# Performance work log

Measured on AMD Instinct MI355X. Metric: run time of the kernel, lower is better.

## Reference

```python
import jax, jax.numpy as jnp
import numpy as np

B, T, IN, H, OUT = 16384, 200, 9, 64, 3


def setup_inputs() -> dict:
    key = jax.random.key(0)
    ks = jax.random.split(key, 12)
    s_in, s_h = 1.0 / np.sqrt(H), 1.0 / np.sqrt(H)  # torch LSTMCell init scale = 1/sqrt(hidden)
    u = lambda k, shape: jax.random.uniform(k, shape, jnp.float32, -s_h, s_h)
    return {
        "x": jax.random.normal(ks[0], (B, T, IN), jnp.float32),
        "W_ih1": u(ks[1], (4 * H, IN)),
        "W_hh1": u(ks[2], (4 * H, H)),
        "b_ih1": u(ks[3], (4 * H,)),
        "b_hh1": u(ks[4], (4 * H,)),
        "W_ih2": u(ks[5], (4 * H, H)),
        "W_hh2": u(ks[6], (4 * H, H)),
        "b_ih2": u(ks[7], (4 * H,)),
        "b_hh2": u(ks[8], (4 * H,)),
        "W_out": u(ks[9], (OUT, H)),
        "b_out": u(ks[10], (OUT,)),
    }


def _lstm_cell(x, h, c, W_ih, W_hh, b_ih, b_hh):
    # PyTorch gate order: i, f, g, o
    gates = x @ W_ih.T + b_ih + h @ W_hh.T + b_hh  # [B, 4H]
    i, f, g, o = jnp.split(gates, 4, axis=-1)
    i, f, o = jax.nn.sigmoid(i), jax.nn.sigmoid(f), jax.nn.sigmoid(o)
    g = jnp.tanh(g)
    c_new = f * c + i * g
    h_new = o * jnp.tanh(c_new)
    return h_new, c_new


def reference(x, W_ih1, W_hh1, b_ih1, b_hh1, W_ih2, W_hh2, b_ih2, b_hh2, W_out, b_out):
    batch = x.shape[0]
    hdim = W_hh1.shape[1]
    zeros = jnp.zeros((batch, hdim), x.dtype)
    init = (zeros, zeros, zeros, zeros)  # h1, c1, h2, c2

    def step(carry, x_t):
        h1, c1, h2, c2 = carry
        h1, c1 = _lstm_cell(x_t, h1, c1, W_ih1, W_hh1, b_ih1, b_hh1)
        h2, c2 = _lstm_cell(h1, h2, c2, W_ih2, W_hh2, b_ih2, b_hh2)
        return (h1, c1, h2, c2), None

    (h1, c1, h2, c2), _ = jax.lax.scan(step, init, jnp.swapaxes(x, 0, 1))  # scan over time
    out = h2 @ W_out.T + b_out  # [B, OUT]
    return out[:, None, :]  # [B, 1, OUT]
```

## Files before the change

### kernel.cpp

```cpp
#include <hip/hip_runtime.h>
#include <hip/hip_bf16.h>


#define B_TOT   16384
#define T_STEPS 200
#define IN_DIM  9
#define HDIM    64

#define PK1_OFF 0
#define PK2_OFF 24576
#define BSUM_HALF_OFF 57344
#define PACK_W_TOT 57344
#define PACK_TOT (PACK_W_TOT + 512)

#define L2E     1.44269504089f
#define TWOL2E  2.88539008178f

typedef _Float16 half8  __attribute__((ext_vector_type(8)));
typedef _Float16 half4v __attribute__((ext_vector_type(4)));
typedef float    f32x4  __attribute__((ext_vector_type(4)));
typedef float    f4u    __attribute__((ext_vector_type(4), aligned(4)));

__global__ void pack_kernel(const float* __restrict__ Wih1, const float* __restrict__ Whh1,
                            const float* __restrict__ bih1, const float* __restrict__ bhh1,
                            const float* __restrict__ Wih2, const float* __restrict__ Whh2,
                            const float* __restrict__ bih2, const float* __restrict__ bhh2,
                            float* __restrict__ ws) {
    int e = blockIdx.x * 256 + threadIdx.x;
    if (e >= PACK_TOT) return;
    _Float16* wh = (_Float16*)ws;
    float* bptr = (float*)(wh + BSUM_HALF_OFF);
    auto gscale = [](int q) -> float {
        int gt = q >> 6;
        return (gt == 2) ? (-2.0f * L2E) : -L2E;
    };
    if (e < PK2_OFF) {
        int j = e & 7, lane = (e >> 3) & 63, nt = (e >> 9) & 15, c = e >> 13;
        int k = c * 32 + 4 * (lane >> 4) + (j & 3) + 16 * (j >> 2);
        int q = nt * 16 + (lane & 15);
        float v = 0.0f;
        if (k < 64)      v = Whh1[q * 64 + k];
        else if (k < 73) v = Wih1[q * 9 + (k - 64)];
        wh[e] = (_Float16)(v * gscale(q));
    } else if (e < PACK_W_TOT) {
        int e2 = e - PK2_OFF;
        int j = e2 & 7, lane = (e2 >> 3) & 63, nt = (e2 >> 9) & 15, c = e2 >> 13;
        int k = c * 32 + 4 * (lane >> 4) + (j & 3) + 16 * (j >> 2);
        int q = nt * 16 + (lane & 15);
        float v = (k < 64) ? Wih2[q * 64 + k] : Whh2[q * 64 + (k - 64)];
        wh[e] = (_Float16)(v * gscale(q));
    } else if (e < PACK_W_TOT + 256) {
        int q = e - PACK_W_TOT;
        bptr[q] = (bih1[q] + bhh1[q]) * gscale(q);
    } else {
        int q = e - PACK_W_TOT - 256;
        bptr[256 + q] = (bih2[q] + bhh2[q]) * gscale(q);
    }
}

__global__ __launch_bounds__(256, 2) void lstm_mfma(
    const float* __restrict__ x,
    const float* __restrict__ ws_f,
    const float* __restrict__ Wout,
    const float* __restrict__ bout,
    float* __restrict__ out)
{
    const int tid  = threadIdx.x;
    const int lane = tid & 63;
    const int w    = __builtin_amdgcn_readfirstlane(tid >> 6);
    const int l15  = lane & 15;
    const int l4   = lane >> 4;

    const _Float16* wh  = (const _Float16*)ws_f;
    const _Float16* pk1 = wh + PK1_OFF;
    const _Float16* pk2 = wh + PK2_OFF;
    const float* bsum   = (const float*)(wh + BSUM_HALF_OFF);

    __shared__ _Float16 h1s[2][16][72];
    __shared__ _Float16 h2s[2][16][72];
    __shared__ _Float16 xwin[2][8][4][16][4];

    for (int i = tid; i < 2 * 16 * 72; i += 256) {
        (&h1s[0][0][0])[i] = (_Float16)0.0f;
        (&h2s[0][0][0])[i] = (_Float16)0.0f;
    }
    for (int i = tid; i < 2 * 8 * 4 * 16 * 4; i += 256)
        (&xwin[0][0][0][0][0])[i] = (_Float16)0.0f;

    const int bbase = blockIdx.x * 16;

    const int b_ = tid & 15, z_ = tid >> 4;
    const int s0_ = (z_ * 11) >> 5, q0_ = z_ - 3 * s0_;
    const bool act1 = (z_ < 8);
    const int pz1 = z_ + 16;
    const int s1_ = (pz1 * 11) >> 5, q1_ = pz1 - 3 * s1_;
    const float* xbL = x + (long)(bbase + b_) * (T_STEPS * IN_DIM);

    f4u pfA = {0.f, 0.f, 0.f, 0.f}, pfB = {0.f, 0.f, 0.f, 0.f};
    auto fetch_x = [&](int wb) {
        int t0 = wb + s0_; if (t0 > T_STEPS - 1) t0 = T_STEPS - 1;
        const float* p0 = xbL + t0 * IN_DIM + 4 * q0_;
        if (q0_ < 2) pfA = *(const f4u*)p0; else pfA[0] = p0[0];
        if (act1) {
            int t1 = wb + s1_; if (t1 > T_STEPS - 1) t1 = T_STEPS - 1;
            const float* p1 = xbL + t1 * IN_DIM + 4 * q1_;
            if (q1_ < 2) pfB = *(const f4u*)p1; else pfB[0] = p1[0];
        }
    };
    auto store_x = [&](int buf) {
        f4u A = pfA, B = pfB;
        if (q0_ == 2) { A[1] = 0.f; A[2] = 0.f; A[3] = 0.f; }
        half4v hv;
        hv[0] = (_Float16)A[0]; hv[1] = (_Float16)A[1];
        hv[2] = (_Float16)A[2]; hv[3] = (_Float16)A[3];
        *(half4v*)&xwin[buf][s0_][q0_][b_][0] = hv;
        if (act1) {
            if (q1_ == 2) { B[1] = 0.f; B[2] = 0.f; B[3] = 0.f; }
            half4v hw;
            hw[0] = (_Float16)B[0]; hw[1] = (_Float16)B[1];
            hw[2] = (_Float16)B[2]; hw[3] = (_Float16)B[3];
            *(half4v*)&xwin[buf][s1_][q1_][b_][0] = hw;
        }
    };
    auto read_ax = [&](int tt) -> half8 {
        half4v xq = *(const half4v*)&xwin[(tt >> 3) & 1][tt & 7][l4][l15][0];
        return __builtin_shufflevector(xq, xq, 0, 1, 2, 3, 0, 1, 2, 3);
    };

    half8 bw1_00, bw1_01, bw1_02, bw1_03;
    half8 bw1_10, bw1_11, bw1_12, bw1_13;
    half8 bw1_20, bw1_21, bw1_22, bw1_23;
    half8 bw2_00, bw2_01, bw2_02, bw2_03;
    half8 bw2_10, bw2_11, bw2_12, bw2_13;
    half8 bw2_20, bw2_21, bw2_22, bw2_23;
    half8 bw2_30, bw2_31, bw2_32, bw2_33;
    {
        #define LD1(c,g) *(const half8*)(pk1 + (((c * 16) + (w + 4 * g)) * 64 + lane) * 8)
        #define LD2(c,g) *(const half8*)(pk2 + (((c * 16) + (w + 4 * g)) * 64 + lane) * 8)
        bw1_00 = LD1(0,0); bw1_01 = LD1(0,1); bw1_02 = LD1(0,2); bw1_03 = LD1(0,3);
        bw1_10 = LD1(1,0); bw1_11 = LD1(1,1); bw1_12 = LD1(1,2); bw1_13 = LD1(1,3);
        bw1_20 = LD1(2,0); bw1_21 = LD1(2,1); bw1_22 = LD1(2,2); bw1_23 = LD1(2,3);
        bw2_00 = LD2(0,0); bw2_01 = LD2(0,1); bw2_02 = LD2(0,2); bw2_03 = LD2(0,3);
        bw2_10 = LD2(1,0); bw2_11 = LD2(1,1); bw2_12 = LD2(1,2); bw2_13 = LD2(1,3);
        bw2_20 = LD2(2,0); bw2_21 = LD2(2,1); bw2_22 = LD2(2,2); bw2_23 = LD2(2,3);
        bw2_30 = LD2(3,0); bw2_31 = LD2(3,1); bw2_32 = LD2(3,2); bw2_33 = LD2(3,3);
        #undef LD1
        #undef LD2
    }

    float bias1[4], bias2[4];
    #pragma unroll
    for (int g = 0; g < 4; ++g) {
        bias1[g] = bsum[(w + 4 * g) * 16 + l15];
        bias2[g] = bsum[256 + (w + 4 * g) * 16 + l15];
    }

    const int hpos = ((w >> 1) << 5) + 8 * (l15 >> 2) + (l15 & 3) + ((w & 1) << 2);

    f32x4 c1 = {0.f, 0.f, 0.f, 0.f};
    f32x4 c2 = {0.f, 0.f, 0.f, 0.f};

    auto cell_update = [&](f32x4* G, f32x4& cs, _Float16* hb) {
        float num[4], den[4], eo4[4], d2[4], hs4[4];
        #pragma unroll
        for (int r = 0; r < 4; ++r) {
            float ei = __builtin_amdgcn_exp2f(G[0][r]);
            float ef = __builtin_amdgcn_exp2f(G[1][r]);
            float eg = __builtin_amdgcn_exp2f(G[2][r]);
            eo4[r]   = __builtin_amdgcn_exp2f(G[3][r]);
            float ai = 1.0f + ei, af = 1.0f + ef, ag = 1.0f + eg;
            float gm = 1.0f - eg;
            float pp = ai * ag;
            num[r] = __builtin_fmaf(gm, af, cs[r] * pp);
            den[r] = af * pp;
        }
        float s01 = den[0] * den[1], s23 = den[2] * den[3];
        float Pinv = __builtin_amdgcn_rcpf(s01 * s23);
        float r01 = Pinv * s23, r23 = Pinv * s01;
        float inv0 = r01 * den[1], inv1 = r01 * den[0];
        float inv2 = r23 * den[3], inv3 = r23 * den[2];
        float inv[4] = {inv0, inv1, inv2, inv3};
        #pragma unroll
        for (int r = 0; r < 4; ++r) {
            float cc = num[r] * inv[r];
            cs[r] = cc;
            float z  = cc * TWOL2E;
            int   zi = __float_as_int(z);
            float ec = __builtin_amdgcn_exp2f(__int_as_float(zi | (int)0x80000000));
            float tm = 1.0f - ec;
            d2[r] = (1.0f + eo4[r]) * (1.0f + ec);
            hs4[r] = __int_as_float(__float_as_int(tm) ^ (zi & (int)0x80000000));
        }
        float t01 = d2[0] * d2[1], t23 = d2[2] * d2[3];
        float Qinv = __builtin_amdgcn_rcpf(t01 * t23);
        float q01 = Qinv * t23, q23 = Qinv * t01;
        float jnv[4] = {q01 * d2[1], q01 * d2[0], q23 * d2[3], q23 * d2[2]};
        #pragma unroll
        for (int r = 0; r < 4; ++r)
            hb[(4 * l4 + r) * 72 + hpos] = (_Float16)(hs4[r] * jnv[r]);
    };

    #define PIN_ALL() do {                                                      \
        asm volatile("" :                                                       \
            "+v"(bw1_00), "+v"(bw1_01), "+v"(bw1_02), "+v"(bw1_03),             \
            "+v"(bw1_10), "+v"(bw1_11), "+v"(bw1_12), "+v"(bw1_13),             \
            "+v"(bw1_20), "+v"(bw1_21), "+v"(bw1_22), "+v"(bw1_23));            \
        asm volatile("" :                                                       \
            "+v"(bw2_00), "+v"(bw2_01), "+v"(bw2_02), "+v"(bw2_03),             \
            "+v"(bw2_10), "+v"(bw2_11), "+v"(bw2_12), "+v"(bw2_13),             \
            "+v"(bw2_20), "+v"(bw2_21), "+v"(bw2_22), "+v"(bw2_23),             \
            "+v"(bw2_30), "+v"(bw2_31), "+v"(bw2_32), "+v"(bw2_33),             \
            "+v"(bias1[0]), "+v"(bias1[1]), "+v"(bias1[2]), "+v"(bias1[3]),     \
            "+v"(bias2[0]), "+v"(bias2[1]), "+v"(bias2[2]), "+v"(bias2[3]));    \
    } while (0)

    fetch_x(0);
    __syncthreads();
    store_x(0);
    fetch_x(8);
    __syncthreads();

    f32x4 C[4];
    {
        half8 ax0 = read_ax(0);
        #pragma unroll
        for (int g = 0; g < 4; ++g) C[g] = (f32x4){bias1[g], bias1[g], bias1[g], bias1[g]};
        C[0] = __builtin_amdgcn_mfma_f32_16x16x32_f16(ax0, bw1_20, C[0], 0, 0, 0);
        C[1] = __builtin_amdgcn_mfma_f32_16x16x32_f16(ax0, bw1_21, C[1], 0, 0, 0);
        C[2] = __builtin_amdgcn_mfma_f32_16x16x32_f16(ax0, bw1_22, C[2], 0, 0, 0);
        C[3] = __builtin_amdgcn_mfma_f32_16x16x32_f16(ax0, bw1_23, C[3], 0, 0, 0);
    }

    for (int t = 0; t < T_STEPS; t += 2) {
        PIN_ALL();
        cell_update(C, c1, &h1s[1][0][0]);
        if ((t & 7) == 0) {
            store_x(((t >> 3) + 1) & 1);
            fetch_x(t + 16);
        }
        __syncthreads();

        half8 a10  = *(const half8*)&h1s[1][l15][ 0 + 8 * l4];
        half8 a11  = *(const half8*)&h1s[1][l15][32 + 8 * l4];
        half8 a2h0 = *(const half8*)&h2s[0][l15][ 0 + 8 * l4];
        half8 a2h1 = *(const half8*)&h2s[0][l15][32 + 8 * l4];
        half8 ax   = read_ax(t + 1);

        f32x4 D[4];
        #pragma unroll
        for (int g = 0; g < 4; ++g) D[g] = (f32x4){bias2[g], bias2[g], bias2[g], bias2[g]};
        D[0] = __builtin_amdgcn_mfma_f32_16x16x32_f16(a10,  bw2_00, D[0], 0, 0, 0);
        D[1] = __builtin_amdgcn_mfma_f32_16x16x32_f16(a10,  bw2_01, D[1], 0, 0, 0);
        D[2] = __builtin_amdgcn_mfma_f32_16x16x32_f16(a10,  bw2_02, D[2], 0, 0, 0);
        D[3] = __builtin_amdgcn_mfma_f32_16x16x32_f16(a10,  bw2_03, D[3], 0, 0, 0);
        D[0] = __builtin_amdgcn_mfma_f32_16x16x32_f16(a11,  bw2_10, D[0], 0, 0, 0);
        D[1] = __builtin_amdgcn_mfma_f32_16x16x32_f16(a11,  bw2_11, D[1], 0, 0, 0);
        D[2] = __builtin_amdgcn_mfma_f32_16x16x32_f16(a11,  bw2_12, D[2], 0, 0, 0);
        D[3] = __builtin_amdgcn_mfma_f32_16x16x32_f16(a11,  bw2_13, D[3], 0, 0, 0);
        D[0] = __builtin_amdgcn_mfma_f32_16x16x32_f16(a2h0, bw2_20, D[0], 0, 0, 0);
        D[1] = __builtin_amdgcn_mfma_f32_16x16x32_f16(a2h0, bw2_21, D[1], 0, 0, 0);
        D[2] = __builtin_amdgcn_mfma_f32_16x16x32_f16(a2h0, bw2_22, D[2], 0, 0, 0);
        D[3] = __builtin_amdgcn_mfma_f32_16x16x32_f16(a2h0, bw2_23, D[3], 0, 0, 0);
        D[0] = __builtin_amdgcn_mfma_f32_16x16x32_f16(a2h1, bw2_30, D[0], 0, 0, 0);
        D[1] = __builtin_amdgcn_mfma_f32_16x16x32_f16(a2h1, bw2_31, D[1], 0, 0, 0);
        D[2] = __builtin_amdgcn_mfma_f32_16x16x32_f16(a2h1, bw2_32, D[2], 0, 0, 0);
        D[3] = __builtin_amdgcn_mfma_f32_16x16x32_f16(a2h1, bw2_33, D[3], 0, 0, 0);

        f32x4 CB[4];
        #pragma unroll
        for (int g = 0; g < 4; ++g) CB[g] = (f32x4){bias1[g], bias1[g], bias1[g], bias1[g]};
        CB[0] = __builtin_amdgcn_mfma_f32_16x16x32_f16(a10, bw1_00, CB[0], 0, 0, 0);
        CB[1] = __builtin_amdgcn_mfma_f32_16x16x32_f16(a10, bw1_01, CB[1], 0, 0, 0);
        CB[2] = __builtin_amdgcn_mfma_f32_16x16x32_f16(a10, bw1_02, CB[2], 0, 0, 0);
        CB[3] = __builtin_amdgcn_mfma_f32_16x16x32_f16(a10, bw1_03, CB[3], 0, 0, 0);
        CB[0] = __builtin_amdgcn_mfma_f32_16x16x32_f16(a11, bw1_10, CB[0], 0, 0, 0);
        CB[1] = __builtin_amdgcn_mfma_f32_16x16x32_f16(a11, bw1_11, CB[1], 0, 0, 0);
        CB[2] = __builtin_amdgcn_mfma_f32_16x16x32_f16(a11, bw1_12, CB[2], 0, 0, 0);
        CB[3] = __builtin_amdgcn_mfma_f32_16x16x32_f16(a11, bw1_13, CB[3], 0, 0, 0);
        CB[0] = __builtin_amdgcn_mfma_f32_16x16x32_f16(ax,  bw1_20, CB[0], 0, 0, 0);
        CB[1] = __builtin_amdgcn_mfma_f32_16x16x32_f16(ax,  bw1_21, CB[1], 0, 0, 0);
        CB[2] = __builtin_amdgcn_mfma_f32_16x16x32_f16(ax,  bw1_22, CB[2], 0, 0, 0);
        CB[3] = __builtin_amdgcn_mfma_f32_16x16x32_f16(ax,  bw1_23, CB[3], 0, 0, 0);

        cell_update(D, c2, &h2s[1][0][0]);

        PIN_ALL();
        cell_update(CB, c1, &h1s[0][0][0]);
        __syncthreads();

        half8 b10  = *(const half8*)&h1s[0][l15][ 0 + 8 * l4];
        half8 b11  = *(const half8*)&h1s[0][l15][32 + 8 * l4];
        half8 b2h0 = *(const half8*)&h2s[1][l15][ 0 + 8 * l4];
        half8 b2h1 = *(const half8*)&h2s[1][l15][32 + 8 * l4];
        half8 bx   = read_ax(t + 2);

        f32x4 E[4];
        #pragma unroll
        for (int g = 0; g < 4; ++g) E[g] = (f32x4){bias2[g], bias2[g], bias2[g], bias2[g]};
        E[0] = __builtin_amdgcn_mfma_f32_16x16x32_f16(b10,  bw2_00, E[0], 0, 0, 0);
        E[1] = __builtin_amdgcn_mfma_f32_16x16x32_f16(b10,  bw2_01, E[1], 0, 0, 0);
        E[2] = __builtin_amdgcn_mfma_f32_16x16x32_f16(b10,  bw2_02, E[2], 0, 0, 0);
        E[3] = __builtin_amdgcn_mfma_f32_16x16x32_f16(b10,  bw2_03, E[3], 0, 0, 0);
        E[0] = __builtin_amdgcn_mfma_f32_16x16x32_f16(b11,  bw2_10, E[0], 0, 0, 0);
        E[1] = __builtin_amdgcn_mfma_f32_16x16x32_f16(b11,  bw2_11, E[1], 0, 0, 0);
        E[2] = __builtin_amdgcn_mfma_f32_16x16x32_f16(b11,  bw2_12, E[2], 0, 0, 0);
        E[3] = __builtin_amdgcn_mfma_f32_16x16x32_f16(b11,  bw2_13, E[3], 0, 0, 0);
        E[0] = __builtin_amdgcn_mfma_f32_16x16x32_f16(b2h0, bw2_20, E[0], 0, 0, 0);
        E[1] = __builtin_amdgcn_mfma_f32_16x16x32_f16(b2h0, bw2_21, E[1], 0, 0, 0);
        E[2] = __builtin_amdgcn_mfma_f32_16x16x32_f16(b2h0, bw2_22, E[2], 0, 0, 0);
        E[3] = __builtin_amdgcn_mfma_f32_16x16x32_f16(b2h0, bw2_23, E[3], 0, 0, 0);
        E[0] = __builtin_amdgcn_mfma_f32_16x16x32_f16(b2h1, bw2_30, E[0], 0, 0, 0);
        E[1] = __builtin_amdgcn_mfma_f32_16x16x32_f16(b2h1, bw2_31, E[1], 0, 0, 0);
        E[2] = __builtin_amdgcn_mfma_f32_16x16x32_f16(b2h1, bw2_32, E[2], 0, 0, 0);
        E[3] = __builtin_amdgcn_mfma_f32_16x16x32_f16(b2h1, bw2_33, E[3], 0, 0, 0);

        #pragma unroll
        for (int g = 0; g < 4; ++g) C[g] = (f32x4){bias1[g], bias1[g], bias1[g], bias1[g]};
        C[0] = __builtin_amdgcn_mfma_f32_16x16x32_f16(b10, bw1_00, C[0], 0, 0, 0);
        C[1] = __builtin_amdgcn_mfma_f32_16x16x32_f16(b10, bw1_01, C[1], 0, 0, 0);
        C[2] = __builtin_amdgcn_mfma_f32_16x16x32_f16(b10, bw1_02, C[2], 0, 0, 0);
        C[3] = __builtin_amdgcn_mfma_f32_16x16x32_f16(b10, bw1_03, C[3], 0, 0, 0);
        C[0] = __builtin_amdgcn_mfma_f32_16x16x32_f16(b11, bw1_10, C[0], 0, 0, 0);
        C[1] = __builtin_amdgcn_mfma_f32_16x16x32_f16(b11, bw1_11, C[1], 0, 0, 0);
        C[2] = __builtin_amdgcn_mfma_f32_16x16x32_f16(b11, bw1_12, C[2], 0, 0, 0);
        C[3] = __builtin_amdgcn_mfma_f32_16x16x32_f16(b11, bw1_13, C[3], 0, 0, 0);
        C[0] = __builtin_amdgcn_mfma_f32_16x16x32_f16(bx,  bw1_20, C[0], 0, 0, 0);
        C[1] = __builtin_amdgcn_mfma_f32_16x16x32_f16(bx,  bw1_21, C[1], 0, 0, 0);
        C[2] = __builtin_amdgcn_mfma_f32_16x16x32_f16(bx,  bw1_22, C[2], 0, 0, 0);
        C[3] = __builtin_amdgcn_mfma_f32_16x16x32_f16(bx,  bw1_23, C[3], 0, 0, 0);

        cell_update(E, c2, &h2s[0][0][0]);
    }
    __syncthreads();

    if (tid < 48) {
        int bl = tid / 3, o = tid - bl * 3;
        float acc = bout[o];
        #pragma unroll 8
        for (int pos = 0; pos < HDIM; ++pos) {
            int sub = pos & 31;
            int j = (pos >> 5) * 32 + (((sub >> 2) & 1) << 4) + ((sub >> 3) << 2) + (sub & 3);
            acc = __builtin_fmaf(Wout[o * 64 + j], (float)h2s[0][bl][pos], acc);
        }
        out[(bbase + bl) * 3 + o] = acc;
    }
    #undef PIN_ALL
}

extern "C" void kernel_launch(void* const* d_in, const int* in_sizes, int n_in,
                              void* d_out, int out_size, void* d_ws, size_t ws_size,
                              hipStream_t stream) {
    const float* x     = (const float*)d_in[0];
    const float* Wih1  = (const float*)d_in[1];
    const float* Whh1  = (const float*)d_in[2];
    const float* bih1  = (const float*)d_in[3];
    const float* bhh1  = (const float*)d_in[4];
    const float* Wih2  = (const float*)d_in[5];
    const float* Whh2  = (const float*)d_in[6];
    const float* bih2  = (const float*)d_in[7];
    const float* bhh2  = (const float*)d_in[8];
    const float* Wout  = (const float*)d_in[9];
    const float* bout  = (const float*)d_in[10];
    float* ws  = (float*)d_ws;
    float* out = (float*)d_out;

    pack_kernel<<<(PACK_TOT + 255) / 256, 256, 0, stream>>>(
        Wih1, Whh1, bih1, bhh1, Wih2, Whh2, bih2, bhh2, ws);

    lstm_mfma<<<B_TOT / 16, 256, 0, stream>>>(x, ws, Wout, bout, out);
}
```

Baseline: 526.4 us.

## Process two independent 16-row batch tiles per block to interleave recurrences

Each block now handles 32 batch rows as two independent 16-row tiles (P and Q) with separate shared-memory state. Their MFMA chains and cell updates are interleaved so one tile's latency-bound recurrence overlaps the other's. The weights held in registers are shared by both tiles, which halves the grid size and the per-row barrier count. s_setprio is also raised around the MFMA sections. The cost is more registers and LDS per block and fewer blocks to spread across CUs, which may reduce occupancy.

```diff
diff --git a/kernel.cpp b/kernel.cpp
--- a/kernel.cpp
+++ b/kernel.cpp
@@ -76,54 +76,58 @@
     const _Float16* pk2 = wh + PK2_OFF;
     const float* bsum   = (const float*)(wh + BSUM_HALF_OFF);
 
-    __shared__ _Float16 h1s[2][16][72];
-    __shared__ _Float16 h2s[2][16][72];
-    __shared__ _Float16 xwin[2][8][4][16][4];
+    __shared__ _Float16 h1P[2][16][72], h2P[2][16][72];
+    __shared__ _Float16 h1Q[2][16][72], h2Q[2][16][72];
+    __shared__ _Float16 xwP[2][8][4][16][4], xwQ[2][8][4][16][4];
 
     for (int i = tid; i < 2 * 16 * 72; i += 256) {
-        (&h1s[0][0][0])[i] = (_Float16)0.0f;
-        (&h2s[0][0][0])[i] = (_Float16)0.0f;
-    }
-    for (int i = tid; i < 2 * 8 * 4 * 16 * 4; i += 256)
-        (&xwin[0][0][0][0][0])[i] = (_Float16)0.0f;
-
-    const int bbase = blockIdx.x * 16;
+        (&h1P[0][0][0])[i] = (_Float16)0.0f; (&h2P[0][0][0])[i] = (_Float16)0.0f;
+        (&h1Q[0][0][0])[i] = (_Float16)0.0f; (&h2Q[0][0][0])[i] = (_Float16)0.0f;
+    }
+    for (int i = tid; i < 2 * 8 * 4 * 16 * 4; i += 256) {
+        (&xwP[0][0][0][0][0])[i] = (_Float16)0.0f;
+        (&xwQ[0][0][0][0][0])[i] = (_Float16)0.0f;
+    }
+
+    const int bbase = blockIdx.x * 32;
 
     const int b_ = tid & 15, z_ = tid >> 4;
     const int s0_ = (z_ * 11) >> 5, q0_ = z_ - 3 * s0_;
     const bool act1 = (z_ < 8);
     const int pz1 = z_ + 16;
     const int s1_ = (pz1 * 11) >> 5, q1_ = pz1 - 3 * s1_;
-    const float* xbL = x + (long)(bbase + b_) * (T_STEPS * IN_DIM);
-
-    f4u pfA = {0.f, 0.f, 0.f, 0.f}, pfB = {0.f, 0.f, 0.f, 0.f};
-    auto fetch_x = [&](int wb) {
+    const float* xbP = x + (long)(bbase + b_) * (T_STEPS * IN_DIM);
+    const float* xbQ = x + (long)(bbase + 16 + b_) * (T_STEPS * IN_DIM);
+
+    f4u pfPA = {0.f,0.f,0.f,0.f}, pfPB = {0.f,0.f,0.f,0.f};
+    f4u pfQA = {0.f,0.f,0.f,0.f}, pfQB = {0.f,0.f,0.f,0.f};
+
+    auto fetch_t = [&](const float* xb, f4u& A, f4u& B, int wb) {
         int t0 = wb + s0_; if (t0 > T_STEPS - 1) t0 = T_STEPS - 1;
-        const float* p0 = xbL + t0 * IN_DIM + 4 * q0_;
-        if (q0_ < 2) pfA = *(const f4u*)p0; else pfA[0] = p0[0];
+        const float* p0 = xb + t0 * IN_DIM + 4 * q0_;
+        if (q0_ < 2) A = *(const f4u*)p0; else A[0] = p0[0];
         if (act1) {
             int t1 = wb + s1_; if (t1 > T_STEPS - 1) t1 = T_STEPS - 1;
-            const float* p1 = xbL + t1 * IN_DIM + 4 * q1_;
-            if (q1_ < 2) pfB = *(const f4u*)p1; else pfB[0] = p1[0];
-        }
-    };
-    auto store_x = [&](int buf) {
-        f4u A = pfA, B = pfB;
+            const float* p1 = xb + t1 * IN_DIM + 4 * q1_;
+            if (q1_ < 2) B = *(const f4u*)p1; else B[0] = p1[0];
+        }
+    };
+    auto store_t = [&](_Float16 (*xw)[8][4][16][4], f4u A, f4u B, int buf) {
         if (q0_ == 2) { A[1] = 0.f; A[2] = 0.f; A[3] = 0.f; }
         half4v hv;
         hv[0] = (_Float16)A[0]; hv[1] = (_Float16)A[1];
         hv[2] = (_Float16)A[2]; hv[3] = (_Float16)A[3];
-        *(half4v*)&xwin[buf][s0_][q0_][b_][0] = hv;
+        *(half4v*)&xw[buf][s0_][q0_][b_][0] = hv;
         if (act1) {
             if (q1_ == 2) { B[1] = 0.f; B[2] = 0.f; B[3] = 0.f; }
             half4v hw;
             hw[0] = (_Float16)B[0]; hw[1] = (_Float16)B[1];
             hw[2] = (_Float16)B[2]; hw[3] = (_Float16)B[3];
-            *(half4v*)&xwin[buf][s1_][q1_][b_][0] = hw;
-        }
-    };
-    auto read_ax = [&](int tt) -> half8 {
-        half4v xq = *(const half4v*)&xwin[(tt >> 3) & 1][tt & 7][l4][l15][0];
+            *(half4v*)&xw[buf][s1_][q1_][b_][0] = hw;
+        }
+    };
+    auto read_ax = [&](const _Float16 (*xw)[8][4][16][4], int tt) -> half8 {
+        half4v xq = *(const half4v*)&xw[(tt >> 3) & 1][tt & 7][l4][l15][0];
         return __builtin_shufflevector(xq, xq, 0, 1, 2, 3, 0, 1, 2, 3);
     };
 
@@ -157,8 +161,8 @@
 
     const int hpos = ((w >> 1) << 5) + 8 * (l15 >> 2) + (l15 & 3) + ((w & 1) << 2);
 
-    f32x4 c1 = {0.f, 0.f, 0.f, 0.f};
-    f32x4 c2 = {0.f, 0.f, 0.f, 0.f};
+    f32x4 c1P = {0.f,0.f,0.f,0.f}, c2P = {0.f,0.f,0.f,0.f};
+    f32x4 c1Q = {0.f,0.f,0.f,0.f}, c2Q = {0.f,0.f,0.f,0.f};
 
     auto cell_update = [&](f32x4* G, f32x4& cs, _Float16* hb) {
         float num[4], den[4], eo4[4], d2[4], hs4[4];
@@ -177,9 +181,7 @@
         float s01 = den[0] * den[1], s23 = den[2] * den[3];
         float Pinv = __builtin_amdgcn_rcpf(s01 * s23);
         float r01 = Pinv * s23, r23 = Pinv * s01;
-        float inv0 = r01 * den[1], inv1 = r01 * den[0];
-        float inv2 = r23 * den[3], inv3 = r23 * den[2];
-        float inv[4] = {inv0, inv1, inv2, inv3};
+        float inv[4] = {r01 * den[1], r01 * den[0], r23 * den[3], r23 * den[2]};
         #pragma unroll
         for (int r = 0; r < 4; ++r) {
             float cc = num[r] * inv[r];
@@ -198,6 +200,43 @@
         #pragma unroll
         for (int r = 0; r < 4; ++r)
             hb[(4 * l4 + r) * 72 + hpos] = (_Float16)(hs4[r] * jnv[r]);
+    };
+
+    auto initb = [&](f32x4* A, const float* b) {
+        #pragma unroll
+        for (int g = 0; g < 4; ++g) A[g] = (f32x4){b[g], b[g], b[g], b[g]};
+    };
+    auto L2C = [&](f32x4* D, half8 u0, half8 u1, half8 v0, half8 v1) {
+        D[0] = __builtin_amdgcn_mfma_f32_16x16x32_f16(u0, bw2_00, D[0], 0, 0, 0);
+        D[1] = __builtin_amdgcn_mfma_f32_16x16x32_f16(u0, bw2_01, D[1], 0, 0, 0);
+        D[2] = __builtin_amdgcn_mfma_f32_16x16x32_f16(u0, bw2_02, D[2], 0, 0, 0);
+        D[3] = __builtin_amdgcn_mfma_f32_16x16x32_f16(u0, bw2_03, D[3], 0, 0, 0);
+        D[0] = __builtin_amdgcn_mfma_f32_16x16x32_f16(u1, bw2_10, D[0], 0, 0, 0);
+        D[1] = __builtin_amdgcn_mfma_f32_16x16x32_f16(u1, bw2_11, D[1], 0, 0, 0);
+        D[2] = __builtin_amdgcn_mfma_f32_16x16x32_f16(u1, bw2_12, D[2], 0, 0, 0);
+        D[3] = __builtin_amdgcn_mfma_f32_16x16x32_f16(u1, bw2_13, D[3], 0, 0, 0);
+        D[0] = __builtin_amdgcn_mfma_f32_16x16x32_f16(v0, bw2_20, D[0], 0, 0, 0);
+        D[1] = __builtin_amdgcn_mfma_f32_16x16x32_f16(v0, bw2_21, D[1], 0, 0, 0);
+        D[2] = __builtin_amdgcn_mfma_f32_16x16x32_f16(v0, bw2_22, D[2], 0, 0, 0);
+        D[3] = __builtin_amdgcn_mfma_f32_16x16x32_f16(v0, bw2_23, D[3], 0, 0, 0);
+        D[0] = __builtin_amdgcn_mfma_f32_16x16x32_f16(v1, bw2_30, D[0], 0, 0, 0);
+        D[1] = __builtin_amdgcn_mfma_f32_16x16x32_f16(v1, bw2_31, D[1], 0, 0, 0);
+        D[2] = __builtin_amdgcn_mfma_f32_16x16x32_f16(v1, bw2_32, D[2], 0, 0, 0);
+        D[3] = __builtin_amdgcn_mfma_f32_16x16x32_f16(v1, bw2_33, D[3], 0, 0, 0);
+    };
+    auto L1C = [&](f32x4* C, half8 u0, half8 u1, half8 axm) {
+        C[0] = __builtin_amdgcn_mfma_f32_16x16x32_f16(u0, bw1_00, C[0], 0, 0, 0);
+        C[1] = __builtin_amdgcn_mfma_f32_16x16x32_f16(u0, bw1_01, C[1], 0, 0, 0);
+        C[2] = __builtin_amdgcn_mfma_f32_16x16x32_f16(u0, bw1_02, C[2], 0, 0, 0);
+        C[3] = __builtin_amdgcn_mfma_f32_16x16x32_f16(u0, bw1_03, C[3], 0, 0, 0);
+        C[0] = __builtin_amdgcn_mfma_f32_16x16x32_f16(u1, bw1_10, C[0], 0, 0, 0);
+        C[1] = __builtin_amdgcn_mfma_f32_16x16x32_f16(u1, bw1_11, C[1], 0, 0, 0);
+        C[2] = __builtin_amdgcn_mfma_f32_16x16x32_f16(u1, bw1_12, C[2], 0, 0, 0);
+        C[3] = __builtin_amdgcn_mfma_f32_16x16x32_f16(u1, bw1_13, C[3], 0, 0, 0);
+        C[0] = __builtin_amdgcn_mfma_f32_16x16x32_f16(axm, bw1_20, C[0], 0, 0, 0);
+        C[1] = __builtin_amdgcn_mfma_f32_16x16x32_f16(axm, bw1_21, C[1], 0, 0, 0);
+        C[2] = __builtin_amdgcn_mfma_f32_16x16x32_f16(axm, bw1_22, C[2], 0, 0, 0);
+        C[3] = __builtin_amdgcn_mfma_f32_16x16x32_f16(axm, bw1_23, C[3], 0, 0, 0);
     };
 
     #define PIN_ALL() do {                                                      \
@@ -214,133 +253,112 @@
             "+v"(bias2[0]), "+v"(bias2[1]), "+v"(bias2[2]), "+v"(bias2[3]));    \
     } while (0)
 
-    fetch_x(0);
+    fetch_t(xbP, pfPA, pfPB, 0);
+    fetch_t(xbQ, pfQA, pfQB, 0);
     __syncthreads();
-    store_x(0);
-    fetch_x(8);
+    store_t(xwP, pfPA, pfPB, 0);
+    store_t(xwQ, pfQA, pfQB, 0);
+    fetch_t(xbP, pfPA, pfPB, 8);
+    fetch_t(xbQ, pfQA, pfQB, 8);
     __syncthreads();
 
-    f32x4 C[4];
+    f32x4 CP[4], CQ[4];
     {
-        half8 ax0 = read_ax(0);
-        #pragma unroll
-        for (int g = 0; g < 4; ++g) C[g] = (f32x4){bias1[g], bias1[g], bias1[g], bias1[g]};
-        C[0] = __builtin_amdgcn_mfma_f32_16x16x32_f16(ax0, bw1_20, C[0], 0, 0, 0);
-        C[1] = __builtin_amdgcn_mfma_f32_16x16x32_f16(ax0, bw1_21, C[1], 0, 0, 0);
-        C[2] = __builtin_amdgcn_mfma_f32_16x16x32_f16(ax0, bw1_22, C[2], 0, 0, 0);
-        C[3] = __builtin_amdgcn_mfma_f32_16x16x32_f16(ax0, bw1_23, C[3], 0, 0, 0);
+        half8 ax0 = read_ax(xwP, 0);
+        initb(CP, bias1);
+        CP[0] = __builtin_amdgcn_mfma_f32_16x16x32_f16(ax0, bw1_20, CP[0], 0, 0, 0);
+        CP[1] = __builtin_amdgcn_mfma_f32_16x16x32_f16(ax0, bw1_21, CP[1], 0, 0, 0);
+        CP[2] = __builtin_amdgcn_mfma_f32_16x16x32_f16(ax0, bw1_22, CP[2], 0, 0, 0);
+        CP[3] = __builtin_amdgcn_mfma_f32_16x16x32_f16(ax0, bw1_23, CP[3], 0, 0, 0);
+        half8 ax1 = read_ax(xwQ, 0);
+        initb(CQ, bias1);
+        CQ[0] = __builtin_amdgcn_mfma_f32_16x16x32_f16(ax1, bw1_20, CQ[0], 0, 0, 0);
+        CQ[1] = __builtin_amdgcn_mfma_f32_16x16x32_f16(ax1, bw1_21, CQ[1], 0, 0, 0);
+        CQ[2] = __builtin_amdgcn_mfma_f32_16x16x32_f16(ax1, bw1_22, CQ[2], 0, 0, 0);
+        CQ[3] = __builtin_amdgcn_mfma_f32_16x16x32_f16(ax1, bw1_23, CQ[3], 0, 0, 0);
     }
 
     for (int t = 0; t < T_STEPS; t += 2) {
         PIN_ALL();
-        cell_update(C, c1, &h1s[1][0][0]);
+        cell_update(CP, c1P, &h1P[1][0][0]);
+        cell_update(CQ, c1Q, &h1Q[1][0][0]);
         if ((t & 7) == 0) {
-            store_x(((t >> 3) + 1) & 1);
-            fetch_x(t + 16);
+            int nb = ((t >> 3) + 1) & 1;
+            store_t(xwP, pfPA, pfPB, nb);
+            store_t(xwQ, pfQA, pfQB, nb);
+            fetch_t(xbP, pfPA, pfPB, t + 16);
+            fetch_t(xbQ, pfQA, pfQB, t + 16);
         }
         __syncthreads();
-
-        half8 a10  = *(const half8*)&h1s[1][l15][ 0 + 8 * l4];
-        half8 a11  = *(const half8*)&h1s[1][l15][32 + 8 * l4];
-        half8 a2h0 = *(const half8*)&h2s[0][l15][ 0 + 8 * l4];
-        half8 a2h1 = *(const half8*)&h2s[0][l15][32 + 8 * l4];
-        half8 ax   = read_ax(t + 1);
-
-        f32x4 D[4];
-        #pragma unroll
-        for (int g = 0; g < 4; ++g) D[g] = (f32x4){bias2[g], bias2[g], bias2[g], bias2[g]};
-        D[0] = __builtin_amdgcn_mfma_f32_16x16x32_f16(a10,  bw2_00, D[0], 0, 0, 0);
-        D[1] = __builtin_amdgcn_mfma_f32_16x16x32_f16(a10,  bw2_01, D[1], 0, 0, 0);
-        D[2] = __builtin_amdgcn_mfma_f32_16x16x32_f16(a10,  bw2_02, D[2], 0, 0, 0);
-        D[3] = __builtin_amdgcn_mfma_f32_16x16x32_f16(a10,  bw2_03, D[3], 0, 0, 0);
-        D[0] = __builtin_amdgcn_mfma_f32_16x16x32_f16(a11,  bw2_10, D[0], 0, 0, 0);
-        D[1] = __builtin_amdgcn_mfma_f32_16x16x32_f16(a11,  bw2_11, D[1], 0, 0, 0);
-        D[2] = __builtin_amdgcn_mfma_f32_16x16x32_f16(a11,  bw2_12, D[2], 0, 0, 0);
-        D[3] = __builtin_amdgcn_mfma_f32_16x16x32_f16(a11,  bw2_13, D[3], 0, 0, 0);
-        D[0] = __builtin_amdgcn_mfma_f32_16x16x32_f16(a2h0, bw2_20, D[0], 0, 0, 0);
-        D[1] = __builtin_amdgcn_mfma_f32_16x16x32_f16(a2h0, bw2_21, D[1], 0, 0, 0);
-        D[2] = __builtin_amdgcn_mfma_f32_16x16x32_f16(a2h0, bw2_22, D[2], 0, 0, 0);
-        D[3] = __builtin_amdgcn_mfma_f32_16x16x32_f16(a2h0, bw2_23, D[3], 0, 0, 0);
-        D[0] = __builtin_amdgcn_mfma_f32_16x16x32_f16(a2h1, bw2_30, D[0], 0, 0, 0);
-        D[1] = __builtin_amdgcn_mfma_f32_16x16x32_f16(a2h1, bw2_31, D[1], 0, 0, 0);
-        D[2] = __builtin_amdgcn_mfma_f32_16x16x32_f16(a2h1, bw2_32, D[2], 0, 0, 0);
-        D[3] = __builtin_amdgcn_mfma_f32_16x16x32_f16(a2h1, bw2_33, D[3], 0, 0, 0);
-
-        f32x4 CB[4];
-        #pragma unroll
-        for (int g = 0; g < 4; ++g) CB[g] = (f32x4){bias1[g], bias1[g], bias1[g], bias1[g]};
-        CB[0] = __builtin_amdgcn_mfma_f32_16x16x32_f16(a10, bw1_00, CB[0], 0, 0, 0);
-        CB[1] = __builtin_amdgcn_mfma_f32_16x16x32_f16(a10, bw1_01, CB[1], 0, 0, 0);
-        CB[2] = __builtin_amdgcn_mfma_f32_16x16x32_f16(a10, bw1_02, CB[2], 0, 0, 0);
-        CB[3] = __builtin_amdgcn_mfma_f32_16x16x32_f16(a10, bw1_03, CB[3], 0, 0, 0);
-        CB[0] = __builtin_amdgcn_mfma_f32_16x16x32_f16(a11, bw1_10, CB[0], 0, 0, 0);
-        CB[1] = __builtin_amdgcn_mfma_f32_16x16x32_f16(a11, bw1_11, CB[1], 0, 0, 0);
-        CB[2] = __builtin_amdgcn_mfma_f32_16x16x32_f16(a11, bw1_12, CB[2], 0, 0, 0);
-        CB[3] = __builtin_amdgcn_mfma_f32_16x16x32_f16(a11, bw1_13, CB[3], 0, 0, 0);
-        CB[0] = __builtin_amdgcn_mfma_f32_16x16x32_f16(ax,  bw1_20, CB[0], 0, 0, 0);
-        CB[1] = __builtin_amdgcn_mfma_f32_16x16x32_f16(ax,  bw1_21, CB[1], 0, 0, 0);
-        CB[2] = __builtin_amdgcn_mfma_f32_16x16x32_f16(ax,  bw1_22, CB[2], 0, 0, 0);
-        CB[3] = __builtin_amdgcn_mfma_f32_16x16x32_f16(ax,  bw1_23, CB[3], 0, 0, 0);
-
-        cell_update(D, c2, &h2s[1][0][0]);
+        __builtin_amdgcn_s_setprio(1);
+        {
+            half8 u0 = *(const half8*)&h1P[1][l15][ 0 + 8 * l4];
+            half8 u1 = *(const half8*)&h1P[1][l15][32 + 8 * l4];
+            half8 v0 = *(const half8*)&h2P[0][l15][ 0 + 8 * l4];
+            half8 v1 = *(const half8*)&h2P[0][l15][32 + 8 * l4];
+            half8 axm = read_ax(xwP, t + 1);
+            f32x4 D[4]; initb(D, bias2);
+            L2C(D, u0, u1, v0, v1);
+            initb(CP, bias1);
+            L1C(CP, u0, u1, axm);
+            cell_update(D, c2P, &h2P[1][0][0]);
+        }
+        {
+            half8 u0 = *(const half8*)&h1Q[1][l15][ 0 + 8 * l4];
+            half8 u1 = *(const half8*)&h1Q[1][l15][32 + 8 * l4];
+            half8 v0 = *(const half8*)&h2Q[0][l15][ 0 + 8 * l4];
+            half8 v1 = *(const half8*)&h2Q[0][l15][32 + 8 * l4];
+            half8 axm = read_ax(xwQ, t + 1);
+            f32x4 D[4]; initb(D, bias2);
+            L2C(D, u0, u1, v0, v1);
+            initb(CQ, bias1);
+            L1C(CQ, u0, u1, axm);
+            cell_update(D, c2Q, &h2Q[1][0][0]);
+        }
+        __builtin_amdgcn_s_setprio(0);
 
         PIN_ALL();
-        cell_update(CB, c1, &h1s[0][0][0]);
+        cell_update(CP, c1P, &h1P[0][0][0]);
+        cell_update(CQ, c1Q, &h1Q[0][0][0]);
         __syncthreads();
-
-        half8 b10  = *(const half8*)&h1s[0][l15][ 0 + 8 * l4];
-        half8 b11  = *(const half8*)&h1s[0][l15][32 + 8 * l4];
-        half8 b2h0 = *(const half8*)&h2s[1][l15][ 0 + 8 * l4];
-        half8 b2h1 = *(const half8*)&h2s[1][l15][32 + 8 * l4];
-        half8 bx   = read_ax(t + 2);
-
-        f32x4 E[4];
-        #pragma unroll
-        for (int g = 0; g < 4; ++g) E[g] = (f32x4){bias2[g], bias2[g], bias2[g], bias2[g]};
-        E[0] = __builtin_amdgcn_mfma_f32_16x16x32_f16(b10,  bw2_00, E[0], 0, 0, 0);
-        E[1] = __builtin_amdgcn_mfma_f32_16x16x32_f16(b10,  bw2_01, E[1], 0, 0, 0);
-        E[2] = __builtin_amdgcn_mfma_f32_16x16x32_f16(b10,  bw2_02, E[2], 0, 0, 0);
-        E[3] = __builtin_amdgcn_mfma_f32_16x16x32_f16(b10,  bw2_03, E[3], 0, 0, 0);
-        E[0] = __builtin_amdgcn_mfma_f32_16x16x32_f16(b11,  bw2_10, E[0], 0, 0, 0);
-        E[1] = __builtin_amdgcn_mfma_f32_16x16x32_f16(b11,  bw2_11, E[1], 0, 0, 0);
-        E[2] = __builtin_amdgcn_mfma_f32_16x16x32_f16(b11,  bw2_12, E[2], 0, 0, 0);
-        E[3] = __builtin_amdgcn_mfma_f32_16x16x32_f16(b11,  bw2_13, E[3], 0, 0, 0);
-        E[0] = __builtin_amdgcn_mfma_f32_16x16x32_f16(b2h0, bw2_20, E[0], 0, 0, 0);
-        E[1] = __builtin_amdgcn_mfma_f32_16x16x32_f16(b2h0, bw2_21, E[1], 0, 0, 0);
-        E[2] = __builtin_amdgcn_mfma_f32_16x16x32_f16(b2h0, bw2_22, E[2], 0, 0, 0);
-        E[3] = __builtin_amdgcn_mfma_f32_16x16x32_f16(b2h0, bw2_23, E[3], 0, 0, 0);
-        E[0] = __builtin_amdgcn_mfma_f32_16x16x32_f16(b2h1, bw2_30, E[0], 0, 0, 0);
-        E[1] = __builtin_amdgcn_mfma_f32_16x16x32_f16(b2h1, bw2_31, E[1], 0, 0, 0);
-        E[2] = __builtin_amdgcn_mfma_f32_16x16x32_f16(b2h1, bw2_32, E[2], 0, 0, 0);
-        E[3] = __builtin_amdgcn_mfma_f32_16x16x32_f16(b2h1, bw2_33, E[3], 0, 0, 0);
-
-        #pragma unroll
-        for (int g = 0; g < 4; ++g) C[g] = (f32x4){bias1[g], bias1[g], bias1[g], bias1[g]};
-        C[0] = __builtin_amdgcn_mfma_f32_16x16x32_f16(b10, bw1_00, C[0], 0, 0, 0);
-        C[1] = __builtin_amdgcn_mfma_f32_16x16x32_f16(b10, bw1_01, C[1], 0, 0, 0);
-        C[2] = __builtin_amdgcn_mfma_f32_16x16x32_f16(b10, bw1_02, C[2], 0, 0, 0);
-        C[3] = __builtin_amdgcn_mfma_f32_16x16x32_f16(b10, bw1_03, C[3], 0, 0, 0);
-        C[0] = __builtin_amdgcn_mfma_f32_16x16x32_f16(b11, bw1_10, C[0], 0, 0, 0);
-        C[1] = __builtin_amdgcn_mfma_f32_16x16x32_f16(b11, bw1_11, C[1], 0, 0, 0);
-        C[2] = __builtin_amdgcn_mfma_f32_16x16x32_f16(b11, bw1_12, C[2], 0, 0, 0);
-        C[3] = __builtin_amdgcn_mfma_f32_16x16x32_f16(b11, bw1_13, C[3], 0, 0, 0);
-        C[0] = __builtin_amdgcn_mfma_f32_16x16x32_f16(bx,  bw1_20, C[0], 0, 0, 0);
-        C[1] = __builtin_amdgcn_mfma_f32_16x16x32_f16(bx,  bw1_21, C[1], 0, 0, 0);
-        C[2] = __builtin_amdgcn_mfma_f32_16x16x32_f16(bx,  bw1_22, C[2], 0, 0, 0);
-        C[3] = __builtin_amdgcn_mfma_f32_16x16x32_f16(bx,  bw1_23, C[3], 0, 0, 0);
-
-        cell_update(E, c2, &h2s[0][0][0]);
+        __builtin_amdgcn_s_setprio(1);
+        {
+            half8 u0 = *(const half8*)&h1P[0][l15][ 0 + 8 * l4];
+            half8 u1 = *(const half8*)&h1P[0][l15][32 + 8 * l4];
+            half8 v0 = *(const half8*)&h2P[1][l15][ 0 + 8 * l4];
+            half8 v1 = *(const half8*)&h2P[1][l15][32 + 8 * l4];
+            half8 axm = read_ax(xwP, t + 2);
+            f32x4 D[4]; initb(D, bias2);
+            L2C(D, u0, u1, v0, v1);
+            initb(CP, bias1);
+            L1C(CP, u0, u1, axm);
+            cell_update(D, c2P, &h2P[0][0][0]);
+        }
+        {
+            half8 u0 = *(const half8*)&h1Q[0][l15][ 0 + 8 * l4];
+            half8 u1 = *(const half8*)&h1Q[0][l15][32 + 8 * l4];
+            half8 v0 = *(const half8*)&h2Q[1][l15][ 0 + 8 * l4];
+            half8 v1 = *(const half8*)&h2Q[1][l15][32 + 8 * l4];
+            half8 axm = read_ax(xwQ, t + 2);
+            f32x4 D[4]; initb(D, bias2);
+            L2C(D, u0, u1, v0, v1);
+            initb(CQ, bias1);
+            L1C(CQ, u0, u1, axm);
+            cell_update(D, c2Q, &h2Q[0][0][0]);
+        }
+        __builtin_amdgcn_s_setprio(0);
     }
     __syncthreads();
 
-    if (tid < 48) {
+    if (tid < 96) {
         int bl = tid / 3, o = tid - bl * 3;
+        const _Float16* src = (bl < 16) ? &h2P[0][bl][0] : &h2Q[0][bl - 16][0];
         float acc = bout[o];
         #pragma unroll 8
         for (int pos = 0; pos < HDIM; ++pos) {
             int sub = pos & 31;
             int j = (pos >> 5) * 32 + (((sub >> 2) & 1) << 4) + ((sub >> 3) << 2) + (sub & 3);
-            acc = __builtin_fmaf(Wout[o * 64 + j], (float)h2s[0][bl][pos], acc);
+            acc = __builtin_fmaf(Wout[o * 64 + j], (float)src[pos], acc);
         }
         out[(bbase + bl) * 3 + o] = acc;
     }
@@ -367,5 +385,5 @@
     pack_kernel<<<(PACK_TOT + 255) / 256, 256, 0, stream>>>(
         Wih1, Whh1, bih1, bhh1, Wih2, Whh2, bih2, bhh2, ws);
 
-    lstm_mfma<<<B_TOT / 16, 256, 0, stream>>>(x, ws, Wout, bout, out);
+    lstm_mfma<<<B_TOT / 32, 256, 0, stream>>>(x, ws, Wout, bout, out);
 }
```

Measured after the change: 557.4 us. 5.9% more time.
